# Kernel optimization log

Measured on AMD Instinct MI355X. Metric: run time of the kernel, lower is better.

## Reference

```python
import jax, jax.numpy as jnp
import numpy as np

GAMMA = 1.0  # init arg gamma


def setup_inputs() -> dict:
    key = jax.random.key(0)
    ks = jax.random.split(key, 7)
    Bn, C, C_, H = 8, 256, 32, 64
    sc = 1.0 / np.sqrt(C)
    return {
        "x_activation": jax.random.normal(ks[0], (Bn, C, H, H), dtype=jnp.float32),
        "f_w": jax.random.normal(ks[1], (C_, C), dtype=jnp.float32) * sc,
        "f_b": jnp.zeros((C_,), dtype=jnp.float32),
        "g_w": jax.random.normal(ks[2], (C_, C), dtype=jnp.float32) * sc,
        "g_b": jnp.zeros((C_,), dtype=jnp.float32),
        "h_w": jax.random.normal(ks[3], (C, C), dtype=jnp.float32) * sc,
        "h_b": jnp.zeros((C,), dtype=jnp.float32),
    }


def reference(x_activation, f_w, f_b, g_w, g_b, h_w, h_b):
    Bn, C, H, W = x_activation.shape
    N = H * W
    xf = x_activation.reshape(Bn, C, N)  # [B, C, N]
    # 1x1 convs are per-pixel linear maps over channels
    f = jnp.einsum('oc,bcn->bon', f_w, xf) + f_b[:, None]  # [B, C_, N]
    g = jnp.einsum('oc,bcn->bon', g_w, xf) + g_b[:, None]  # [B, C_, N]
    h = jnp.einsum('oc,bcn->bon', h_w, xf) + h_b[:, None]  # [B, C, N]
    # S[b, i, j] = sum_c f[b, c, i] * g[b, c, j]  (f^T @ g), shape [B, N, N]
    S = jnp.einsum('bci,bcj->bij', f, g)
    # NOTE: original uses Softmax(dim=1) -> normalize over the i (query/f) axis
    B = jax.nn.softmax(S, axis=1)
    # O (post-transpose) [b, c, i] = sum_j B[b, i, j] * h[b, c, j]
    O = jnp.einsum('bij,bcj->bci', B, h).reshape(Bn, C, H, W)
    return GAMMA * O + x_activation
```

## Files before the change

kernel.cpp:

```cpp
#include <hip/hip_runtime.h>
#include <hip/hip_fp16.h>
#include <cmath>


#define BN 8
#define CC 256
#define CQ 32
#define NN 4096

typedef _Float16 half8 __attribute__((ext_vector_type(8)));
typedef _Float16 half4v __attribute__((ext_vector_type(4)));
typedef float f32x4 __attribute__((ext_vector_type(4)));

static __device__ __forceinline__ float fexp2(float x) {
    return __builtin_amdgcn_exp2f(x);
}

#define LOG2E 1.44269504f
#define SHIFT2 28.8539008f

__global__ __launch_bounds__(256) void cvtw_kernel(
    const float* __restrict__ fw, const float* __restrict__ gw,
    const float* __restrict__ hw, __half* __restrict__ wf16)
{
    int i = blockIdx.x * 256 + threadIdx.x;
    float v;
    if (i < 8192)       v = fw[i];
    else if (i < 16384) v = gw[i - 8192];
    else                v = hw[i - 16384];
    wf16[i] = __float2half(v);
}

__global__ __launch_bounds__(256) void tp_proj_kernel(
    const float* __restrict__ x, const __half* __restrict__ wf16,
    const float* __restrict__ fb, const float* __restrict__ gb,
    const float* __restrict__ hb,
    __half* __restrict__ ft, __half* __restrict__ gt, __half* __restrict__ hm)
{
    const int tid = threadIdx.x;
    const int w = tid >> 6, lane = tid & 63, col = lane & 15, q = lane >> 4;
    const int gid = blockIdx.x;
    const int b  = gid & 7;
    const int n0 = (gid >> 3) * 64;

    __shared__ float  T[64 * 65];
    __shared__ __half XT[64 * 256];

    const int u  = tid >> 4;
    const int n4 = (tid & 15) * 4;
    const int nn = w * 16 + (lane >> 2);
    const int cc = (lane & 3) * 16;
    const int sA = 8 * (nn & 7);

    f32x4 vx[4][4];
    const float* xb = x + (size_t)b * CC * NN + n0;
#pragma unroll
    for (int c4 = 0; c4 < 4; ++c4)
#pragma unroll
        for (int r = 0; r < 4; ++r)
            vx[c4][r] = __builtin_nontemporal_load(
                (const f32x4*)(xb + (size_t)(c4 * 64 + r * 16 + u) * NN + n4));

#pragma unroll
    for (int c4 = 0; c4 < 4; ++c4) {
        const int c0 = c4 * 64;
#pragma unroll
        for (int r = 0; r < 4; ++r) {
            int c = r * 16 + u;
            T[c * 65 + n4 + 0] = vx[c4][r].x;
            T[c * 65 + n4 + 1] = vx[c4][r].y;
            T[c * 65 + n4 + 2] = vx[c4][r].z;
            T[c * 65 + n4 + 3] = vx[c4][r].w;
        }
        __syncthreads();
        half8 o0, o1;
#pragma unroll
        for (int k = 0; k < 8; ++k) {
            o0[k] = (_Float16)T[(cc + k) * 65 + nn];
            o1[k] = (_Float16)T[(cc + 8 + k) * 65 + nn];
        }
        *(half8*)(void*)(&XT[nn * 256 + ((c0 + cc) ^ sA)])     = o0;
        *(half8*)(void*)(&XT[nn * 256 + ((c0 + cc + 8) ^ sA)]) = o1;
        __syncthreads();
    }

    const f32x4 zero = {0.f, 0.f, 0.f, 0.f};
    const int sw = 8 * (col & 7);

    {
        const __half* fw16 = wf16;
        const __half* gw16 = wf16 + 8192;
        f32x4 acc[4];
#pragma unroll
        for (int mt = 0; mt < 4; ++mt) acc[mt] = zero;
        const int pixl = 16 * w + col;
#pragma unroll
        for (int ks = 0; ks < 8; ++ks) {
            half8 bf = *(const half8*)(const void*)(
                &XT[pixl * 256 + ((ks * 32 + q * 8) ^ sw)]);
#pragma unroll
            for (int mt = 0; mt < 4; ++mt) {
                const __half* wp = (mt < 2) ? (fw16 + (16 * mt + col) * CC)
                                            : (gw16 + (16 * (mt - 2) + col) * CC);
                half8 af = *(const half8*)(const void*)(wp + ks * 32 + q * 8);
                acc[mt] = __builtin_amdgcn_mfma_f32_16x16x32_f16(af, bf, acc[mt], 0, 0, 0);
            }
        }
        const int pix = n0 + pixl;
#pragma unroll
        for (int mt = 0; mt < 4; ++mt) {
            const int mtl = mt & 1;
            const float* bsel = (mt < 2) ? fb : gb;
            __half* dsel = (mt < 2) ? ft : gt;
            half4v hv;
#pragma unroll
            for (int r = 0; r < 4; ++r)
                hv[r] = (_Float16)(acc[mt][r] + bsel[16 * mtl + 4 * q + r]);
            *(half4v*)(void*)(dsel + ((size_t)b * NN + pix) * CQ + 16 * mtl + 4 * q) = hv;
        }
    }

    {
        const __half* hw16 = wf16 + 16384;
        f32x4 acc[4][4];
#pragma unroll
        for (int mt = 0; mt < 4; ++mt)
#pragma unroll
            for (int ci = 0; ci < 4; ++ci) acc[mt][ci] = zero;
#pragma unroll
        for (int ks = 0; ks < 8; ++ks) {
            half8 af[4], bf[4];
#pragma unroll
            for (int mt = 0; mt < 4; ++mt)
                af[mt] = *(const half8*)(const void*)(
                    &XT[(16 * mt + col) * 256 + ((ks * 32 + q * 8) ^ sw)]);
#pragma unroll
            for (int ci = 0; ci < 4; ++ci)
                bf[ci] = *(const half8*)(const void*)(
                    hw16 + (size_t)(16 * (4 * w + ci) + col) * CC + ks * 32 + q * 8);
#pragma unroll
            for (int mt = 0; mt < 4; ++mt)
#pragma unroll
                for (int ci = 0; ci < 4; ++ci)
                    acc[mt][ci] = __builtin_amdgcn_mfma_f32_16x16x32_f16(
                        af[mt], bf[ci], acc[mt][ci], 0, 0, 0);
        }
#pragma unroll
        for (int ci = 0; ci < 4; ++ci) {
            const int c = 16 * (4 * w + ci) + col;
            const float bias = hb[c];
#pragma unroll
            for (int mt = 0; mt < 4; ++mt) {
                half4v hv;
#pragma unroll
                for (int r = 0; r < 4; ++r)
                    hv[r] = (_Float16)(acc[mt][ci][r] + bias);
                *(half4v*)(void*)(hm + ((size_t)b * CC + c) * NN + n0 + 16 * mt + 4 * q) = hv;
            }
        }
    }
}

__global__ __launch_bounds__(256) void pass1a_kernel(
    const __half* __restrict__ ft, const __half* __restrict__ gt,
    float* __restrict__ lpart)
{
    const int tid = threadIdx.x;
    const int w = tid >> 6, lane = tid & 63, col = lane & 15, q = lane >> 4;
    const int gid = blockIdx.x;
    const int b  = gid & 7;
    const int jt = (gid >> 3) & 63;
    const int iq = gid >> 9;
    const int jg = jt * 64 + 16 * w + col;
    const int ibase = iq * 1024;

    const __half* fbase = ft + (size_t)b * NN * CQ;
    half8 gfrag = *(const half8*)(const void*)(gt + ((size_t)b * NN + jg) * CQ + q * 8);

    float a0 = 0.f, a1 = 0.f, a2 = 0.f, a3 = 0.f;
    const f32x4 zero = {0.f, 0.f, 0.f, 0.f};

    half8 a0v = *(const half8*)(const void*)(fbase + (size_t)(ibase + col) * CQ + q * 8);
    half8 a1v = *(const half8*)(const void*)(fbase + (size_t)(ibase + 16 + col) * CQ + q * 8);
    for (int t = 0; t < 32; ++t) {
        int i_n = ibase + ((t + 1) & 31) * 32;
        half8 a2v = *(const half8*)(const void*)(fbase + (size_t)(i_n + col) * CQ + q * 8);
        half8 a3v = *(const half8*)(const void*)(fbase + (size_t)(i_n + 16 + col) * CQ + q * 8);
        f32x4 d0 = __builtin_amdgcn_mfma_f32_16x16x32_f16(a0v, gfrag, zero, 0, 0, 0);
        f32x4 d1 = __builtin_amdgcn_mfma_f32_16x16x32_f16(a1v, gfrag, zero, 0, 0, 0);
        a0 += fexp2(fmaf(d0[0], LOG2E, -SHIFT2)) + fexp2(fmaf(d1[0], LOG2E, -SHIFT2));
        a1 += fexp2(fmaf(d0[1], LOG2E, -SHIFT2)) + fexp2(fmaf(d1[1], LOG2E, -SHIFT2));
        a2 += fexp2(fmaf(d0[2], LOG2E, -SHIFT2)) + fexp2(fmaf(d1[2], LOG2E, -SHIFT2));
        a3 += fexp2(fmaf(d0[3], LOG2E, -SHIFT2)) + fexp2(fmaf(d1[3], LOG2E, -SHIFT2));
        a0v = a2v;
        a1v = a3v;
    }
    float l = (a0 + a1) + (a2 + a3);
    l += __shfl_xor(l, 16);
    l += __shfl_xor(l, 32);
    if (q == 0)
        lpart[((size_t)iq * BN + b) * NN + jg] = l;
}

__global__ __launch_bounds__(256) void pass1b_kernel(
    const float* __restrict__ lpart, float* __restrict__ shl)
{
    const int i4 = (blockIdx.x * 256 + threadIdx.x) * 4;
    f32x4 s0 = *(const f32x4*)(lpart + i4);
    f32x4 s1 = *(const f32x4*)(lpart + 1 * BN * NN + i4);
    f32x4 s2 = *(const f32x4*)(lpart + 2 * BN * NN + i4);
    f32x4 s3 = *(const f32x4*)(lpart + 3 * BN * NN + i4);
    f32x4 o;
    o.x = -__log2f((s0.x + s1.x) + (s2.x + s3.x)) - SHIFT2;
    o.y = -__log2f((s0.y + s1.y) + (s2.y + s3.y)) - SHIFT2;
    o.z = -__log2f((s0.z + s1.z) + (s2.z + s3.z)) - SHIFT2;
    o.w = -__log2f((s0.w + s1.w) + (s2.w + s3.w)) - SHIFT2;
    *(f32x4*)(shl + i4) = o;
}

__global__ __launch_bounds__(256, 2) void pass2_kernel(
    const float* __restrict__ x,
    const __half* __restrict__ ft, const __half* __restrict__ gt,
    const __half* __restrict__ hm, const float* __restrict__ shl,
    float* __restrict__ out)
{
    const int tid = threadIdx.x;
    const int w = tid >> 6, lane = tid & 63, col = lane & 15, q = lane >> 4;
    const int gid = blockIdx.x;
    const int b  = gid & 7;
    const int i0 = (gid >> 3) * 64;
    const int cb = 64 * w;

    __shared__ __half P[2][64 * 64];

    const __half* gbase = gt + (size_t)b * NN * CQ;
    const __half* hbase = hm + (size_t)b * CC * NN;
    const float*  lb    = shl + (size_t)b * NN;

    half8 ffr[4];
#pragma unroll
    for (int it = 0; it < 4; ++it)
        ffr[it] = *(const half8*)(const void*)(ft + ((size_t)b * NN + i0 + 16 * it + col) * CQ + q * 8);

    f32x4 acc[4][4];
#pragma unroll
    for (int ms = 0; ms < 4; ++ms)
#pragma unroll
        for (int ns = 0; ns < 4; ++ns)
            acc[ms][ns] = (f32x4){0.f, 0.f, 0.f, 0.f};

    const f32x4 zero = {0.f, 0.f, 0.f, 0.f};
    const int jml = 16 * w + 4 * q;
    const int sw  = 8 * (col & 7);

    half8 gfr = *(const half8*)(const void*)(gbase + (size_t)(16 * w + col) * CQ + q * 8);
    f32x4 sl  = *(const f32x4*)(lb + jml);

    int buf = 0;
    for (int j0 = 0; j0 < NN; j0 += 64, buf ^= 1) {
        half8 hv[4][2];
#pragma unroll
        for (int ns = 0; ns < 4; ++ns)
#pragma unroll
            for (int ks = 0; ks < 2; ++ks)
                hv[ns][ks] = *(const half8*)(const void*)(
                    hbase + (size_t)(cb + 16 * ns + col) * NN + j0 + ks * 32 + q * 8);

        f32x4 d[4];
#pragma unroll
        for (int it = 0; it < 4; ++it)
            d[it] = __builtin_amdgcn_mfma_f32_16x16x32_f16(gfr, ffr[it], zero, 0, 0, 0);

        const int jn = (j0 + 64) & (NN - 1);
        half8 gfr_n = *(const half8*)(const void*)(gbase + (size_t)(jn + 16 * w + col) * CQ + q * 8);
        f32x4 sl_n  = *(const f32x4*)(lb + jn + jml);

        __half* Pb = &P[buf][0];
#pragma unroll
        for (int it = 0; it < 4; ++it) {
            half4v pv;
            pv[0] = (_Float16)fexp2(fmaf(d[it][0], LOG2E, sl[0]));
            pv[1] = (_Float16)fexp2(fmaf(d[it][1], LOG2E, sl[1]));
            pv[2] = (_Float16)fexp2(fmaf(d[it][2], LOG2E, sl[2]));
            pv[3] = (_Float16)fexp2(fmaf(d[it][3], LOG2E, sl[3]));
            *(half4v*)(void*)(Pb + (16 * it + col) * 64 + (jml ^ sw)) = pv;
        }
        __syncthreads();

#pragma unroll
        for (int ks = 0; ks < 2; ++ks) {
            half8 af[4];
#pragma unroll
            for (int ms = 0; ms < 4; ++ms)
                af[ms] = *(const half8*)(const void*)(
                    Pb + (16 * ms + col) * 64 + ((ks * 32 + q * 8) ^ sw));
#pragma unroll
            for (int ms = 0; ms < 4; ++ms)
#pragma unroll
                for (int ns = 0; ns < 4; ++ns)
                    acc[ms][ns] = __builtin_amdgcn_mfma_f32_16x16x32_f16(
                        af[ms], hv[ns][ks], acc[ms][ns], 0, 0, 0);
        }
        gfr = gfr_n;
        sl  = sl_n;
    }

    const float* xb = x + (size_t)b * CC * NN;
    float* ob = out + (size_t)b * CC * NN;
#pragma unroll
    for (int ms = 0; ms < 4; ++ms) {
#pragma unroll
        for (int ns = 0; ns < 4; ++ns) {
            int c  = cb + 16 * ns + col;
            int ii = i0 + 16 * ms + 4 * q;
            size_t off = (size_t)c * NN + ii;
            f32x4 xv = __builtin_nontemporal_load((const f32x4*)(xb + off));
            f32x4 ov;
            ov.x = acc[ms][ns][0] + xv.x;
            ov.y = acc[ms][ns][1] + xv.y;
            ov.z = acc[ms][ns][2] + xv.z;
            ov.w = acc[ms][ns][3] + xv.w;
            __builtin_nontemporal_store(ov, (f32x4*)(ob + off));
        }
    }
}

extern "C" void kernel_launch(void* const* d_in, const int* in_sizes, int n_in,
                              void* d_out, int out_size, void* d_ws, size_t ws_size,
                              hipStream_t stream)
{
    const float* x  = (const float*)d_in[0];
    const float* fw = (const float*)d_in[1];
    const float* fb = (const float*)d_in[2];
    const float* gw = (const float*)d_in[3];
    const float* gb = (const float*)d_in[4];
    const float* hw = (const float*)d_in[5];
    const float* hb = (const float*)d_in[6];
    float* out = (float*)d_out;

    char* ws = (char*)d_ws;
    __half* wf = (__half*)(ws);
    __half* ft = (__half*)(ws + (size_t)262144);
    __half* gt = (__half*)(ws + (size_t)2359296);
    __half* hm = (__half*)(ws + (size_t)4456448);
    float*  lv = (float*) (ws + (size_t)21233664);
    float*  lp = (float*) (ws + (size_t)21364736);

    cvtw_kernel<<<dim3(320), dim3(256), 0, stream>>>(fw, gw, hw, wf);
    tp_proj_kernel<<<dim3(512), dim3(256), 0, stream>>>(x, wf, fb, gb, hb, ft, gt, hm);
    pass1a_kernel<<<dim3(2048), dim3(256), 0, stream>>>(ft, gt, lp);
    pass1b_kernel<<<dim3(32), dim3(256), 0, stream>>>(lp, lv);
    pass2_kernel<<<dim3(512), dim3(256), 0, stream>>>(x, ft, gt, hm, lv, out);
}
```

Baseline: 289.8 us.

## Fuse weight conversion and softmax-normalizer reduction into consumer kernels

```diff
diff --git a/kernel.cpp b/kernel.cpp
--- a/kernel.cpp
+++ b/kernel.cpp
@@ -7,6 +7,7 @@
 #define CC 256
 #define CQ 32
 #define NN 4096
+#define LPSTEP (BN * NN)
 
 typedef _Float16 half8 __attribute__((ext_vector_type(8)));
 typedef _Float16 half4v __attribute__((ext_vector_type(4)));
@@ -19,20 +20,34 @@
 #define LOG2E 1.44269504f
 #define SHIFT2 28.8539008f
 
-__global__ __launch_bounds__(256) void cvtw_kernel(
+static __device__ __forceinline__ f32x4 load_sl(const float* lp, int off) {
+    f32x4 s0 = *(const f32x4*)(lp + off);
+    f32x4 s1 = *(const f32x4*)(lp + LPSTEP + off);
+    f32x4 s2 = *(const f32x4*)(lp + 2 * LPSTEP + off);
+    f32x4 s3 = *(const f32x4*)(lp + 3 * LPSTEP + off);
+    f32x4 o;
+    o.x = -__log2f((s0.x + s1.x) + (s2.x + s3.x)) - SHIFT2;
+    o.y = -__log2f((s0.y + s1.y) + (s2.y + s3.y)) - SHIFT2;
+    o.z = -__log2f((s0.z + s1.z) + (s2.z + s3.z)) - SHIFT2;
+    o.w = -__log2f((s0.w + s1.w) + (s2.w + s3.w)) - SHIFT2;
+    return o;
+}
+
+static __device__ __forceinline__ half8 ldcvt8(const float* p) {
+    f32x4 v0 = *(const f32x4*)(p);
+    f32x4 v1 = *(const f32x4*)(p + 4);
+    half8 h;
+    h[0] = (_Float16)v0.x; h[1] = (_Float16)v0.y;
+    h[2] = (_Float16)v0.z; h[3] = (_Float16)v0.w;
+    h[4] = (_Float16)v1.x; h[5] = (_Float16)v1.y;
+    h[6] = (_Float16)v1.z; h[7] = (_Float16)v1.w;
+    return h;
+}
+
+__global__ __launch_bounds__(256) void tp_proj_kernel(
+    const float* __restrict__ x,
     const float* __restrict__ fw, const float* __restrict__ gw,
-    const float* __restrict__ hw, __half* __restrict__ wf16)
-{
-    int i = blockIdx.x * 256 + threadIdx.x;
-    float v;
-    if (i < 8192)       v = fw[i];
-    else if (i < 16384) v = gw[i - 8192];
-    else                v = hw[i - 16384];
-    wf16[i] = __float2half(v);
-}
-
-__global__ __launch_bounds__(256) void tp_proj_kernel(
-    const float* __restrict__ x, const __half* __restrict__ wf16,
+    const float* __restrict__ hw,
     const float* __restrict__ fb, const float* __restrict__ gb,
     const float* __restrict__ hb,
     __half* __restrict__ ft, __half* __restrict__ gt, __half* __restrict__ hm)
@@ -88,8 +103,6 @@
     const int sw = 8 * (col & 7);
 
     {
-        const __half* fw16 = wf16;
-        const __half* gw16 = wf16 + 8192;
         f32x4 acc[4];
 #pragma unroll
         for (int mt = 0; mt < 4; ++mt) acc[mt] = zero;
@@ -100,9 +113,9 @@
                 &XT[pixl * 256 + ((ks * 32 + q * 8) ^ sw)]);
 #pragma unroll
             for (int mt = 0; mt < 4; ++mt) {
-                const __half* wp = (mt < 2) ? (fw16 + (16 * mt + col) * CC)
-                                            : (gw16 + (16 * (mt - 2) + col) * CC);
-                half8 af = *(const half8*)(const void*)(wp + ks * 32 + q * 8);
+                const float* wp = (mt < 2) ? (fw + (size_t)(16 * mt + col) * CC)
+                                           : (gw + (size_t)(16 * (mt - 2) + col) * CC);
+                half8 af = ldcvt8(wp + ks * 32 + q * 8);
                 acc[mt] = __builtin_amdgcn_mfma_f32_16x16x32_f16(af, bf, acc[mt], 0, 0, 0);
             }
         }
@@ -121,7 +134,6 @@
     }
 
     {
-        const __half* hw16 = wf16 + 16384;
         f32x4 acc[4][4];
 #pragma unroll
         for (int mt = 0; mt < 4; ++mt)
@@ -136,8 +148,7 @@
                     &XT[(16 * mt + col) * 256 + ((ks * 32 + q * 8) ^ sw)]);
 #pragma unroll
             for (int ci = 0; ci < 4; ++ci)
-                bf[ci] = *(const half8*)(const void*)(
-                    hw16 + (size_t)(16 * (4 * w + ci) + col) * CC + ks * 32 + q * 8);
+                bf[ci] = ldcvt8(hw + (size_t)(16 * (4 * w + ci) + col) * CC + ks * 32 + q * 8);
 #pragma unroll
             for (int mt = 0; mt < 4; ++mt)
 #pragma unroll
@@ -202,26 +213,10 @@
         lpart[((size_t)iq * BN + b) * NN + jg] = l;
 }
 
-__global__ __launch_bounds__(256) void pass1b_kernel(
-    const float* __restrict__ lpart, float* __restrict__ shl)
-{
-    const int i4 = (blockIdx.x * 256 + threadIdx.x) * 4;
-    f32x4 s0 = *(const f32x4*)(lpart + i4);
-    f32x4 s1 = *(const f32x4*)(lpart + 1 * BN * NN + i4);
-    f32x4 s2 = *(const f32x4*)(lpart + 2 * BN * NN + i4);
-    f32x4 s3 = *(const f32x4*)(lpart + 3 * BN * NN + i4);
-    f32x4 o;
-    o.x = -__log2f((s0.x + s1.x) + (s2.x + s3.x)) - SHIFT2;
-    o.y = -__log2f((s0.y + s1.y) + (s2.y + s3.y)) - SHIFT2;
-    o.z = -__log2f((s0.z + s1.z) + (s2.z + s3.z)) - SHIFT2;
-    o.w = -__log2f((s0.w + s1.w) + (s2.w + s3.w)) - SHIFT2;
-    *(f32x4*)(shl + i4) = o;
-}
-
 __global__ __launch_bounds__(256, 2) void pass2_kernel(
     const float* __restrict__ x,
     const __half* __restrict__ ft, const __half* __restrict__ gt,
-    const __half* __restrict__ hm, const float* __restrict__ shl,
+    const __half* __restrict__ hm, const float* __restrict__ lpart,
     float* __restrict__ out)
 {
     const int tid = threadIdx.x;
@@ -235,7 +230,7 @@
 
     const __half* gbase = gt + (size_t)b * NN * CQ;
     const __half* hbase = hm + (size_t)b * CC * NN;
-    const float*  lb    = shl + (size_t)b * NN;
+    const float*  lb    = lpart + (size_t)b * NN;
 
     half8 ffr[4];
 #pragma unroll
@@ -254,7 +249,7 @@
     const int sw  = 8 * (col & 7);
 
     half8 gfr = *(const half8*)(const void*)(gbase + (size_t)(16 * w + col) * CQ + q * 8);
-    f32x4 sl  = *(const f32x4*)(lb + jml);
+    f32x4 sl  = load_sl(lb, jml);
 
     int buf = 0;
     for (int j0 = 0; j0 < NN; j0 += 64, buf ^= 1) {
@@ -273,7 +268,7 @@
 
         const int jn = (j0 + 64) & (NN - 1);
         half8 gfr_n = *(const half8*)(const void*)(gbase + (size_t)(jn + 16 * w + col) * CQ + q * 8);
-        f32x4 sl_n  = *(const f32x4*)(lb + jn + jml);
+        f32x4 sl_n  = load_sl(lb, jn + jml);
 
         __half* Pb = &P[buf][0];
 #pragma unroll
@@ -339,16 +334,12 @@
     float* out = (float*)d_out;
 
     char* ws = (char*)d_ws;
-    __half* wf = (__half*)(ws);
-    __half* ft = (__half*)(ws + (size_t)262144);
-    __half* gt = (__half*)(ws + (size_t)2359296);
-    __half* hm = (__half*)(ws + (size_t)4456448);
-    float*  lv = (float*) (ws + (size_t)21233664);
-    float*  lp = (float*) (ws + (size_t)21364736);
-
-    cvtw_kernel<<<dim3(320), dim3(256), 0, stream>>>(fw, gw, hw, wf);
-    tp_proj_kernel<<<dim3(512), dim3(256), 0, stream>>>(x, wf, fb, gb, hb, ft, gt, hm);
+    __half* ft = (__half*)(ws);
+    __half* gt = (__half*)(ws + (size_t)2097152);
+    __half* hm = (__half*)(ws + (size_t)4194304);
+    float*  lp = (float*) (ws + (size_t)20971520);
+
+    tp_proj_kernel<<<dim3(512), dim3(256), 0, stream>>>(x, fw, gw, hw, fb, gb, hb, ft, gt, hm);
     pass1a_kernel<<<dim3(2048), dim3(256), 0, stream>>>(ft, gt, lp);
-    pass1b_kernel<<<dim3(32), dim3(256), 0, stream>>>(lp, lv);
-    pass2_kernel<<<dim3(512), dim3(256), 0, stream>>>(x, ft, gt, hm, lv, out);
-}
+    pass2_kernel<<<dim3(512), dim3(256), 0, stream>>>(x, ft, gt, hm, lp, out);
+}
```

New measurement: 311.6 us. 7.5% more time.
